# Kernel tuning notes

Measured on AMD Instinct MI355X. Metric: run time of the kernel, lower is better.

Reference implementation:

```python
import jax, jax.numpy as jnp
import numpy as np

N, E, G = 50000, 800000, 512
IN_DIM, HID, HEADS = 128, 32, 4
NEG_SLOPE = 0.2


def _gat_conv(x, W, a_src, a_dst, b, src, dst, heads, ch):
    # x: [N, F_in]; W: [F_in, heads*ch]; a_src/a_dst: [heads, ch]; b: [heads*ch]
    h = (x @ W).reshape(N, heads, ch)                      # [N,H,C]
    alpha_s = jnp.einsum('nhc,hc->nh', h, a_src)           # [N,H]
    alpha_d = jnp.einsum('nhc,hc->nh', h, a_dst)           # [N,H]
    e = jax.nn.leaky_relu(alpha_s[src] + alpha_d[dst], NEG_SLOPE)  # [E,H]
    # scatter-softmax over incoming edges of each destination node
    m = jax.ops.segment_max(e, dst, num_segments=N)        # [N,H]
    ex = jnp.exp(e - m[dst])
    denom = jax.ops.segment_sum(ex, dst, num_segments=N)   # [N,H]
    alpha = ex / (denom[dst] + 1e-16)                      # [E,H]
    msg = h[src] * alpha[:, :, None]                       # [E,H,C]
    out = jax.ops.segment_sum(msg, dst, num_segments=N)    # [N,H,C]
    return out.reshape(N, heads * ch) + b


def _forward(x, edge_index, batch_idx, params):
    # PyG GATConv default: add self-loops
    loops = jnp.arange(N, dtype=edge_index.dtype)
    src = jnp.concatenate([edge_index[0], loops])
    dst = jnp.concatenate([edge_index[1], loops])
    heads_per_layer = [(HEADS, HID), (HEADS, HID), (1, HID)]
    h = x
    for (W, a_s, a_d, b), (hh, cc) in zip(params, heads_per_layer):
        h = _gat_conv(h, W, a_s, a_d, b, src, dst, hh, cc)
        h = jax.nn.elu(h)  # dropout is identity in eval mode
    # global mean pool over graphs
    sums = jax.ops.segment_sum(h, batch_idx, num_segments=G)          # [G,HID]
    cnts = jax.ops.segment_sum(jnp.ones((N,), h.dtype), batch_idx, num_segments=G)
    return sums / jnp.maximum(cnts, 1.0)[:, None]


def setup_inputs() -> dict:
    key = jax.random.key(0)
    ks = jax.random.split(key, 16)
    x = jax.random.normal(ks[0], (N, IN_DIM), dtype=jnp.float32)
    edge_index = jax.random.randint(ks[1], (2, E), 0, N, dtype=jnp.int32)
    batch_idx = jnp.sort(jax.random.randint(ks[2], (N,), 0, G, dtype=jnp.int32))
    dims = [(IN_DIM, HEADS, HID), (HEADS * HID, HEADS, HID), (HEADS * HID, 1, HID)]
    inp = {'x': x, 'edge_index': edge_index, 'batch_idx': batch_idx}
    for i, (fin, hh, cc) in enumerate(dims, 1):
        s = 1.0 / np.sqrt(fin)
        inp[f'W{i}'] = jax.random.normal(ks[3 * i], (fin, hh * cc), jnp.float32) * s
        inp[f'as{i}'] = jax.random.normal(ks[3 * i + 1], (hh, cc), jnp.float32) * 0.1
        inp[f'ad{i}'] = jax.random.normal(ks[3 * i + 2], (hh, cc), jnp.float32) * 0.1
        inp[f'b{i}'] = jnp.zeros((hh * cc,), jnp.float32)
    return inp


def reference(x, edge_index, batch_idx, W1, as1, ad1, b1, W2, as2, ad2, b2, W3, as3, ad3, b3):
    params = [(W1, as1, ad1, b1), (W2, as2, ad2, b2), (W3, as3, ad3, b3)]
    return _forward(x, edge_index, batch_idx, params)
```

## Files before the change

kernel.cpp:

```cpp
#include <hip/hip_runtime.h>
#include <hip/hip_fp16.h>

#define THREADS 256
#define NREG 8
#define CAP 64

__device__ __forceinline__ float lrelu(float x) { return x > 0.f ? x : 0.2f * x; }
__device__ __forceinline__ float elu(float x) { return x > 0.f ? x : expm1f(x); }

template <int K, int H, int C>
__global__ __launch_bounds__(256, 6) void gemm_alpha_kernel(
    const float* __restrict__ X, const float* __restrict__ W,
    const float* __restrict__ a_src, const float* __restrict__ a_dst,
    __half* __restrict__ Hh, float* __restrict__ asb, float* __restrict__ adb, int nNodes) {
    constexpr int M = 128;
    constexpr int NB = 32;
    __shared__ float xs[NB][K + 4];

    const int t = threadIdx.x;
    const int wid = t >> 6;
    const int lane = t & 63;
    const int half = lane >> 5;
    const int lq = lane & 31;
    const int col4 = lq * 4;
    const int node0 = blockIdx.x * NB;
    const int nbase = node0 + wid * 8 + half * 4;

    for (int i = t; i < NB * K; i += THREADS) {
        int n = i >> 7, k = i & (K - 1);
        int gn = node0 + n;
        xs[n][k] = (gn < nNodes) ? X[(size_t)gn * K + k] : 0.f;
    }
    __syncthreads();

    float acc[4][4];
#pragma unroll
    for (int j = 0; j < 4; ++j)
#pragma unroll
        for (int c = 0; c < 4; ++c) acc[j][c] = 0.f;

    const int nloc = wid * 8 + half * 4;
    for (int kg = 0; kg < K; kg += 4) {
        float4 xv[4];
#pragma unroll
        for (int j = 0; j < 4; ++j)
            xv[j] = *reinterpret_cast<const float4*>(&xs[nloc + j][kg]);
        float4 w4[4];
#pragma unroll
        for (int kk = 0; kk < 4; ++kk)
            w4[kk] = *reinterpret_cast<const float4*>(&W[(size_t)(kg + kk) * M + col4]);
#pragma unroll
        for (int kk = 0; kk < 4; ++kk) {
#pragma unroll
            for (int j = 0; j < 4; ++j) {
                float xj = (&xv[j].x)[kk];
                acc[j][0] += xj * w4[kk].x;
                acc[j][1] += xj * w4[kk].y;
                acc[j][2] += xj * w4[kk].z;
                acc[j][3] += xj * w4[kk].w;
            }
        }
    }

#pragma unroll
    for (int j = 0; j < 4; ++j) {
        int gn = nbase + j;
        if (gn < nNodes) {
            __half2 p01 = __floats2half2_rn(acc[j][0], acc[j][1]);
            __half2 p23 = __floats2half2_rn(acc[j][2], acc[j][3]);
            uint2 u = make_uint2(*reinterpret_cast<unsigned*>(&p01),
                                 *reinterpret_cast<unsigned*>(&p23));
            *reinterpret_cast<uint2*>(&Hh[(size_t)gn * M + col4]) = u;
        }
    }

    float as_[4], ad_[4];
#pragma unroll
    for (int c = 0; c < 4; ++c) { as_[c] = a_src[col4 + c]; ad_[c] = a_dst[col4 + c]; }

    float sv[4], dv[4];
#pragma unroll
    for (int j = 0; j < 4; ++j) {
        sv[j] = acc[j][0] * as_[0] + acc[j][1] * as_[1] + acc[j][2] * as_[2] +
                acc[j][3] * as_[3];
        dv[j] = acc[j][0] * ad_[0] + acc[j][1] * ad_[1] + acc[j][2] * ad_[2] +
                acc[j][3] * ad_[3];
    }
#pragma unroll
    for (int off = 1; off < 8; off <<= 1) {
#pragma unroll
        for (int j = 0; j < 4; ++j) {
            sv[j] += __shfl_xor(sv[j], off);
            dv[j] += __shfl_xor(dv[j], off);
        }
    }
    if ((lq & 7) == 0) {
        int h = lq >> 3;
#pragma unroll
        for (int j = 0; j < 4; ++j) {
            int gn = nbase + j;
            if (gn < nNodes) {
                asb[gn * H + h] = sv[j];
                adb[gn * H + h] = dv[j];
            }
        }
    }
}

template <int K>
__global__ void gemm32_alpha_kernel(const float* __restrict__ X, const float* __restrict__ W,
                                    const float* __restrict__ a_src,
                                    const float* __restrict__ a_dst,
                                    __half* __restrict__ Hh, float* __restrict__ asb,
                                    float* __restrict__ adb, int nNodes) {
    constexpr int M = 32;
    constexpr int NB = 16;
    constexpr int NL = THREADS / M;
    constexpr int PER = NB / NL;
    __shared__ float xs[NB][K];

    int node0 = blockIdx.x * NB;
    for (int i = threadIdx.x; i < NB * K; i += THREADS) {
        int nn = i / K, kk = i % K;
        int n = node0 + nn;
        xs[nn][kk] = (n < nNodes) ? X[(size_t)n * K + kk] : 0.f;
    }
    __syncthreads();

    int col = threadIdx.x & 31;
    int nl = threadIdx.x >> 5;
    float acc[PER];
#pragma unroll
    for (int i = 0; i < PER; ++i) acc[i] = 0.f;

    for (int k = 0; k < K; ++k) {
        float w = W[k * M + col];
#pragma unroll
        for (int i = 0; i < PER; ++i) acc[i] += xs[nl + i * NL][k] * w;
    }

    float as = a_src[col], ad = a_dst[col];
#pragma unroll
    for (int i = 0; i < PER; ++i) {
        int n = node0 + nl + i * NL;
        float sv = acc[i] * as, dv = acc[i] * ad;
#pragma unroll
        for (int off = 1; off < 32; off <<= 1) {
            sv += __shfl_xor(sv, off);
            dv += __shfl_xor(dv, off);
        }
        if (n < nNodes) {
            Hh[(size_t)n * M + col] = __float2half(acc[i]);
            if (col == 0) { asb[n] = sv; adb[n] = dv; }
        }
    }
}

__global__ void scatterP_kernel(const int* __restrict__ src, const int* __restrict__ dst,
                                int* __restrict__ cursor, unsigned short* __restrict__ csr,
                                int nE, int N) {
    const int r = blockIdx.x & (NREG - 1);
    const int nb = gridDim.x / NREG;
    const int bi = blockIdx.x / NREG;
    const int span = (N + NREG - 1) / NREG;
    const int lo = r * span;
    const int hi = min(N, lo + span);
    const int stride = nb * THREADS;
    for (int e = bi * THREADS + (int)threadIdx.x; e < nE; e += stride) {
        int d = dst[e];
        if (d >= lo && d < hi) {
            int p = atomicAdd(&cursor[d], 1);
            if (p < CAP) csr[(d << 6) + p] = (unsigned short)src[e];
        }
    }
}

template <int H>
__device__ __forceinline__ void load_t(const float* __restrict__ asb, int s, bool valid,
                                       const float* adn, float* t) {
    if constexpr (H == 4) {
        float4 a4 = reinterpret_cast<const float4*>(asb)[s];
        float v[4] = {a4.x, a4.y, a4.z, a4.w};
#pragma unroll
        for (int h = 0; h < 4; ++h) t[h] = valid ? lrelu(v[h] + adn[h]) : -3.0e38f;
    } else {
        t[0] = valid ? lrelu(asb[s] + adn[0]) : -3.0e38f;
    }
}

template <int M, int H, int C>
__global__ void node_aggr(const __half* __restrict__ Hh, const float* __restrict__ asb,
                          const float* __restrict__ adb, const int* __restrict__ degArr,
                          const unsigned short* __restrict__ csr,
                          const float* __restrict__ bias, float* __restrict__ out,
                          int nNodes) {
    constexpr int WPB = THREADS / 64;
    constexpr int PSTR = (H == 4) ? 5 : 1;
    __shared__ uint2 pair_sh[WPB][64 * PSTR];

    const int wid = threadIdx.x >> 6;
    const int lane = threadIdx.x & 63;
    const int node = blockIdx.x * WPB + wid;
    if (node >= nNodes) return;

    const int e0 = node << 6;
    const int deg = min(degArr[node], CAP);

    float adn[H], eself[H];
    if constexpr (H == 4) {
        float4 ad4 = reinterpret_cast<const float4*>(adb)[node];
        float4 as4 = reinterpret_cast<const float4*>(asb)[node];
        adn[0] = ad4.x; adn[1] = ad4.y; adn[2] = ad4.z; adn[3] = ad4.w;
        eself[0] = lrelu(as4.x + adn[0]);
        eself[1] = lrelu(as4.y + adn[1]);
        eself[2] = lrelu(as4.z + adn[2]);
        eself[3] = lrelu(as4.w + adn[3]);
    } else {
        adn[0] = adb[node];
        eself[0] = lrelu(asb[node] + adn[0]);
    }

    const bool valid = lane < deg;
    const int s = valid ? (int)csr[e0 + lane] : node;
    float t[H];
    load_t<H>(asb, s, valid, adn, t);

    float ex[H], den[H], inv[H];
#pragma unroll
    for (int h = 0; h < H; ++h) { ex[h] = __expf(t[h]); den[h] = ex[h]; }
#pragma unroll
    for (int off = 32; off > 0; off >>= 1)
#pragma unroll
        for (int h = 0; h < H; ++h) den[h] += __shfl_xor(den[h], off);
#pragma unroll
    for (int h = 0; h < H; ++h) {
        den[h] += __expf(eself[h]);
        inv[h] = 1.f / (den[h] + 1e-16f);
    }

    unsigned wo = (unsigned)(s * M);
#pragma unroll
    for (int h = 0; h < H; ++h) {
        float al = ex[h] * inv[h];
        pair_sh[wid][lane * PSTR + h] = make_uint2(wo, __float_as_uint(al));
    }

    if constexpr (M == 128) {
        constexpr int CPL = 2;
        int ch = lane * CPL;
        const int myh = ch / C;

        float ii = inv[0], es = eself[0];
#pragma unroll
        for (int h = 1; h < H; ++h)
            if (myh == h) { ii = inv[h]; es = eself[h]; }

        float acc[2];
        const float alSelf = __expf(es) * ii;
        float2 hv0 = __half22float2(
            *reinterpret_cast<const __half2*>(&Hh[(size_t)node * M + ch]));
        acc[0] = alSelf * hv0.x;
        acc[1] = alSelf * hv0.y;

        int cnt = (deg + 7) & ~7;
        for (int j0 = 0; j0 < cnt; j0 += 8) {
#pragma unroll
            for (int jj = 0; jj < 8; ++jj) {
                int j = j0 + jj;
                uint2 p = pair_sh[wid][j * PSTR + myh];
                float al = __uint_as_float(p.y);
                __half2 h2 = *reinterpret_cast<const __half2*>(&Hh[(int)p.x + ch]);
                float2 hv = __half22float2(h2);
                acc[0] += al * hv.x;
                acc[1] += al * hv.y;
            }
        }

#pragma unroll
        for (int c = 0; c < 2; ++c)
            out[(size_t)node * M + ch + c] = elu(acc[c] + bias[ch + c]);
    } else {
        const int g2 = lane >> 5;
        const int c = lane & 31;
        const float ii = inv[0], es = eself[0];

        float acc = 0.f;
        int cnt = (deg + 15) & ~15;
        for (int j0 = 0; j0 < cnt; j0 += 16) {
#pragma unroll
            for (int jj = 0; jj < 8; ++jj) {
                int j = j0 + jj * 2 + g2;
                uint2 p = pair_sh[wid][j];
                float al = __uint_as_float(p.y);
                acc += al * __half2float(Hh[(int)p.x + c]);
            }
        }

        acc += __shfl_xor(acc, 32);
        if (lane < 32) {
            const float alSelf = __expf(es) * ii;
            float sv = __half2float(Hh[(size_t)node * M + c]);
            out[(size_t)node * M + c] = elu(acc + alSelf * sv + bias[c]);
        }
    }
}

__global__ void pool_kernel(const float* __restrict__ act, const int* __restrict__ batch,
                            float* __restrict__ out, int N, int G) {
    int wid = threadIdx.x >> 6;
    int lane = threadIdx.x & 63;
    int g = blockIdx.x * (THREADS / 64) + wid;
    if (g >= G) return;

    int s, e;
    {
        int lo = 0, hi = N;
        while (lo < hi) { int mid = (lo + hi) >> 1; if (batch[mid] < g) lo = mid + 1; else hi = mid; }
        s = lo;
        hi = N;
        while (lo < hi) { int mid = (lo + hi) >> 1; if (batch[mid] < g + 1) lo = mid + 1; else hi = mid; }
        e = lo;
    }

    int c = lane & 31, half = lane >> 5;
    float acc = 0.f;
    for (int n = s + half; n < e; n += 2) acc += act[(size_t)n * 32 + c];
    acc += __shfl_xor(acc, 32);
    if (lane < 32) out[g * 32 + c] = acc / fmaxf((float)(e - s), 1.f);
}

extern "C" void kernel_launch(void* const* d_in, const int* in_sizes, int n_in, void* d_out,
                              int out_size, void* d_ws, size_t ws_size, hipStream_t stream) {
    const float* x = (const float*)d_in[0];
    const int* ei = (const int*)d_in[1];
    const int* batch = (const int*)d_in[2];
    const float* W1 = (const float*)d_in[3];
    const float* as1 = (const float*)d_in[4];
    const float* ad1 = (const float*)d_in[5];
    const float* b1 = (const float*)d_in[6];
    const float* W2 = (const float*)d_in[7];
    const float* as2 = (const float*)d_in[8];
    const float* ad2 = (const float*)d_in[9];
    const float* b2 = (const float*)d_in[10];
    const float* W3 = (const float*)d_in[11];
    const float* as3 = (const float*)d_in[12];
    const float* ad3 = (const float*)d_in[13];
    const float* b3 = (const float*)d_in[14];

    const int N = in_sizes[0] / 128;
    const int E = in_sizes[1] / 2;
    const int G = out_size / 32;
    const int* srcp = ei;
    const int* dstp = ei + E;

    char* ws = (char*)d_ws;
    float* B = (float*)ws;
    __half* Hh = (__half*)(B + (size_t)N * 128);
    float* asb = (float*)(Hh + (size_t)N * 128);
    float* adb = asb + (size_t)N * 4;
    int* cursor = (int*)(adb + (size_t)N * 4);
    unsigned short* csr = (unsigned short*)(cursor + N);

    const int scatterBlocks = NREG * 256;
    const int gaBlocks = (N + 31) / 32;

    hipMemsetAsync(cursor, 0, (size_t)N * 4, stream);
    scatterP_kernel<<<scatterBlocks, THREADS, 0, stream>>>(srcp, dstp, cursor, csr, E, N);

    gemm_alpha_kernel<128, 4, 32><<<gaBlocks, THREADS, 0, stream>>>(x, W1, as1, ad1, Hh, asb,
                                                                    adb, N);
    node_aggr<128, 4, 32><<<(N + 3) / 4, THREADS, 0, stream>>>(Hh, asb, adb, cursor, csr, b1,
                                                               B, N);
    gemm_alpha_kernel<128, 4, 32><<<gaBlocks, THREADS, 0, stream>>>(B, W2, as2, ad2, Hh, asb,
                                                                    adb, N);
    node_aggr<128, 4, 32><<<(N + 3) / 4, THREADS, 0, stream>>>(Hh, asb, adb, cursor, csr, b2,
                                                               B, N);
    gemm32_alpha_kernel<128><<<(N + 15) / 16, THREADS, 0, stream>>>(B, W3, as3, ad3, Hh, asb,
                                                                    adb, N);
    node_aggr<32, 1, 32><<<(N + 3) / 4, THREADS, 0, stream>>>(Hh, asb, adb, cursor, csr, b3,
                                                              B, N);

    pool_kernel<<<(G + 3) / 4, THREADS, 0, stream>>>(B, batch, (float*)d_out, N, G);
}
```

Baseline: 266.4 us.

## Stage weight matrix in LDS and stream X rows directly in GEMM-alpha kernels

The 128-wide GEMM kernel now loads the whole 128x128 weight matrix into shared memory per block and reads X rows straight from global memory. Each wave computes 4 nodes with 2 columns per lane, and the block size drops to 16 nodes. The 32-wide layer-3 GEMM also stages its weights in LDS instead of reading them from global memory. This trades the per-block X staging for a 64KB weight copy into every block. That limits occupancy and adds a lot of W load traffic, since twice as many blocks each reload W. The last block's node0 is also clamped to N-4 so edge rows get recomputed.

```diff
diff --git a/kernel.cpp b/kernel.cpp
--- a/kernel.cpp
+++ b/kernel.cpp
@@ -9,96 +9,82 @@
 __device__ __forceinline__ float elu(float x) { return x > 0.f ? x : expm1f(x); }
 
 template <int K, int H, int C>
-__global__ __launch_bounds__(256, 6) void gemm_alpha_kernel(
+__global__ __launch_bounds__(256, 2) void gemm_alpha_kernel(
     const float* __restrict__ X, const float* __restrict__ W,
     const float* __restrict__ a_src, const float* __restrict__ a_dst,
     __half* __restrict__ Hh, float* __restrict__ asb, float* __restrict__ adb, int nNodes) {
     constexpr int M = 128;
-    constexpr int NB = 32;
-    __shared__ float xs[NB][K + 4];
+    constexpr int NB = 16;
+    __shared__ float wsh[K][M];
 
     const int t = threadIdx.x;
     const int wid = t >> 6;
     const int lane = t & 63;
-    const int half = lane >> 5;
-    const int lq = lane & 31;
-    const int col4 = lq * 4;
-    const int node0 = blockIdx.x * NB;
-    const int nbase = node0 + wid * 8 + half * 4;
-
-    for (int i = t; i < NB * K; i += THREADS) {
-        int n = i >> 7, k = i & (K - 1);
-        int gn = node0 + n;
-        xs[n][k] = (gn < nNodes) ? X[(size_t)gn * K + k] : 0.f;
-    }
+    const int c2 = lane * 2;
+
+    for (int i = t; i < K * M / 4; i += THREADS)
+        reinterpret_cast<float4*>(&wsh[0][0])[i] = reinterpret_cast<const float4*>(W)[i];
     __syncthreads();
 
-    float acc[4][4];
-#pragma unroll
-    for (int j = 0; j < 4; ++j)
-#pragma unroll
-        for (int c = 0; c < 4; ++c) acc[j][c] = 0.f;
-
-    const int nloc = wid * 8 + half * 4;
+    int node0 = blockIdx.x * NB + wid * 4;
+    if (node0 > nNodes - 4) node0 = nNodes - 4;
+    const float* xrow = X + (size_t)node0 * K;
+
+    float a00 = 0.f, a01 = 0.f, a10 = 0.f, a11 = 0.f;
+    float a20 = 0.f, a21 = 0.f, a30 = 0.f, a31 = 0.f;
+
+#pragma unroll 2
     for (int kg = 0; kg < K; kg += 4) {
-        float4 xv[4];
-#pragma unroll
-        for (int j = 0; j < 4; ++j)
-            xv[j] = *reinterpret_cast<const float4*>(&xs[nloc + j][kg]);
-        float4 w4[4];
-#pragma unroll
-        for (int kk = 0; kk < 4; ++kk)
-            w4[kk] = *reinterpret_cast<const float4*>(&W[(size_t)(kg + kk) * M + col4]);
+        float4 xv0 = *reinterpret_cast<const float4*>(xrow + 0 * K + kg);
+        float4 xv1 = *reinterpret_cast<const float4*>(xrow + 1 * K + kg);
+        float4 xv2 = *reinterpret_cast<const float4*>(xrow + 2 * K + kg);
+        float4 xv3 = *reinterpret_cast<const float4*>(xrow + 3 * K + kg);
 #pragma unroll
         for (int kk = 0; kk < 4; ++kk) {
-#pragma unroll
-            for (int j = 0; j < 4; ++j) {
-                float xj = (&xv[j].x)[kk];
-                acc[j][0] += xj * w4[kk].x;
-                acc[j][1] += xj * w4[kk].y;
-                acc[j][2] += xj * w4[kk].z;
-                acc[j][3] += xj * w4[kk].w;
-            }
-        }
-    }
-
+            float2 w2 = *reinterpret_cast<const float2*>(&wsh[kg + kk][c2]);
+            float x0 = (&xv0.x)[kk];
+            float x1 = (&xv1.x)[kk];
+            float x2 = (&xv2.x)[kk];
+            float x3 = (&xv3.x)[kk];
+            a00 += x0 * w2.x; a01 += x0 * w2.y;
+            a10 += x1 * w2.x; a11 += x1 * w2.y;
+            a20 += x2 * w2.x; a21 += x2 * w2.y;
+            a30 += x3 * w2.x; a31 += x3 * w2.y;
+        }
+    }
+
+    float accj0[4] = {a00, a10, a20, a30};
+    float accj1[4] = {a01, a11, a21, a31};
 #pragma unroll
     for (int j = 0; j < 4; ++j) {
-        int gn = nbase + j;
+        int gn = node0 + j;
         if (gn < nNodes) {
-            __half2 p01 = __floats2half2_rn(acc[j][0], acc[j][1]);
-            __half2 p23 = __floats2half2_rn(acc[j][2], acc[j][3]);
-            uint2 u = make_uint2(*reinterpret_cast<unsigned*>(&p01),
-                                 *reinterpret_cast<unsigned*>(&p23));
-            *reinterpret_cast<uint2*>(&Hh[(size_t)gn * M + col4]) = u;
-        }
-    }
-
-    float as_[4], ad_[4];
-#pragma unroll
-    for (int c = 0; c < 4; ++c) { as_[c] = a_src[col4 + c]; ad_[c] = a_dst[col4 + c]; }
-
+            __half2 p = __floats2half2_rn(accj0[j], accj1[j]);
+            *reinterpret_cast<__half2*>(&Hh[(size_t)gn * M + c2]) = p;
+        }
+    }
+
+    float as0 = a_src[c2], as1 = a_src[c2 + 1];
+    float ad0 = a_dst[c2], ad1 = a_dst[c2 + 1];
     float sv[4], dv[4];
 #pragma unroll
     for (int j = 0; j < 4; ++j) {
-        sv[j] = acc[j][0] * as_[0] + acc[j][1] * as_[1] + acc[j][2] * as_[2] +
-                acc[j][3] * as_[3];
-        dv[j] = acc[j][0] * ad_[0] + acc[j][1] * ad_[1] + acc[j][2] * ad_[2] +
-                acc[j][3] * ad_[3];
-    }
-#pragma unroll
-    for (int off = 1; off < 8; off <<= 1) {
+        sv[j] = accj0[j] * as0 + accj1[j] * as1;
+        dv[j] = accj0[j] * ad0 + accj1[j] * ad1;
+    }
+#pragma unroll
+    for (int off = 1; off < 16; off <<= 1) {
 #pragma unroll
         for (int j = 0; j < 4; ++j) {
             sv[j] += __shfl_xor(sv[j], off);
             dv[j] += __shfl_xor(dv[j], off);
         }
     }
-    if ((lq & 7) == 0) {
-        int h = lq >> 3;
+    if ((lane & 15) == 0) {
+        int h = lane >> 4;
 #pragma unroll
         for (int j = 0; j < 4; ++j) {
-            int gn = nbase + j;
+            int gn = node0 + j;
             if (gn < nNodes) {
                 asb[gn * H + h] = sv[j];
                 adb[gn * H + h] = dv[j];
@@ -118,6 +104,7 @@
     constexpr int NL = THREADS / M;
     constexpr int PER = NB / NL;
     __shared__ float xs[NB][K];
+    __shared__ float w3[K][M];
 
     int node0 = blockIdx.x * NB;
     for (int i = threadIdx.x; i < NB * K; i += THREADS) {
@@ -125,6 +112,8 @@
         int n = node0 + nn;
         xs[nn][kk] = (n < nNodes) ? X[(size_t)n * K + kk] : 0.f;
     }
+    for (int i = threadIdx.x; i < K * M / 4; i += THREADS)
+        reinterpret_cast<float4*>(&w3[0][0])[i] = reinterpret_cast<const float4*>(W)[i];
     __syncthreads();
 
     int col = threadIdx.x & 31;
@@ -134,7 +123,7 @@
     for (int i = 0; i < PER; ++i) acc[i] = 0.f;
 
     for (int k = 0; k < K; ++k) {
-        float w = W[k * M + col];
+        float w = w3[k][col];
 #pragma unroll
         for (int i = 0; i < PER; ++i) acc[i] += xs[nl + i * NL][k] * w;
     }
@@ -362,7 +351,7 @@
     unsigned short* csr = (unsigned short*)(cursor + N);
 
     const int scatterBlocks = NREG * 256;
-    const int gaBlocks = (N + 31) / 32;
+    const int gaBlocks = (N + 15) / 16;
 
     hipMemsetAsync(cursor, 0, (size_t)N * 4, stream);
     scatterP_kernel<<<scatterBlocks, THREADS, 0, stream>>>(srcp, dstp, cursor, csr, E, N);
```

Result: slower. 333.0 us (+25.0%).
